# Performance work log

Hardware: AMD Instinct MI355X
Metric: run time of the kernel (lower is better)

## Reference

```python
import jax, jax.numpy as jnp
import numpy as np

N_NODES = 50000
N_EDGES = 600000
N_LABEL = 200000
IN_CH = 128
OUT_CH = 128
K_HOPS = 2


def setup_inputs() -> dict:
    key = jax.random.key(0)
    ks = jax.random.split(key, 9)
    x = jax.random.normal(ks[0], (N_NODES, IN_CH), dtype=jnp.float32)
    edge_index = jax.random.randint(ks[1], (2, N_EDGES), 0, N_NODES)
    edge_label_index = jax.random.randint(ks[2], (2, N_LABEL), 0, N_NODES)
    conv_weight = jax.random.normal(ks[3], (OUT_CH, IN_CH), dtype=jnp.float32) * 0.05
    conv_bias = jax.random.normal(ks[4], (OUT_CH,), dtype=jnp.float32) * 0.05
    w1 = jax.random.normal(ks[5], (OUT_CH // 2, OUT_CH), dtype=jnp.float32) * 0.05
    b1 = jax.random.normal(ks[6], (OUT_CH // 2,), dtype=jnp.float32) * 0.05
    w2 = jax.random.normal(ks[7], (1, OUT_CH // 2), dtype=jnp.float32) * 0.05
    b2 = jax.random.normal(ks[8], (1,), dtype=jnp.float32) * 0.05
    return {"x": x, "edge_index": edge_index, "edge_label_index": edge_label_index,
            "conv_weight": conv_weight, "conv_bias": conv_bias,
            "w1": w1, "b1": b1, "w2": w2, "b2": b2}


def reference(x, edge_index, edge_label_index, conv_weight, conv_bias, w1, b1, w2, b2):
    n = x.shape[0]
    # gcn_norm with self-loops: A_hat = D^{-1/2} (A + I) D^{-1/2}
    loop = jnp.arange(n, dtype=edge_index.dtype)
    src = jnp.concatenate([edge_index[0], loop])  # message sources
    dst = jnp.concatenate([edge_index[1], loop])  # aggregation targets
    deg = jax.ops.segment_sum(jnp.ones_like(dst, dtype=x.dtype), dst, num_segments=n)
    dinv = jnp.where(deg > 0, jax.lax.rsqrt(deg), 0.0)
    w = dinv[src] * dinv[dst]  # [E+N] edge weights

    # K-hop propagation: h <- A_hat h, repeated K times (SGConv)
    h = x
    for _ in range(K_HOPS):
        h = jax.ops.segment_sum(h[src] * w[:, None], dst, num_segments=n)
    z = h @ conv_weight.T + conv_bias  # [N, out_channels]

    # decode: gather endpoint embeddings, multiply, tiny MLP (dropout inactive at eval)
    s = z[edge_label_index[0]] * z[edge_label_index[1]]  # [E_label, out]
    h1 = jax.nn.relu(s @ w1.T + b1)
    r = (h1 @ w2.T + b2).sum(axis=-1)  # [E_label]
    return r
```

## Files before the change

### kernel.cpp

```cpp
#include <hip/hip_runtime.h>

#define N_CH 128

typedef _Float16 half8  __attribute__((ext_vector_type(8)));
typedef _Float16 half4v __attribute__((ext_vector_type(4)));
typedef float    floatx4 __attribute__((ext_vector_type(4)));


__global__ void k_prep(int* __restrict__ cnt,
                       const float* __restrict__ W,  _Float16* __restrict__ wh,
                       const float* __restrict__ W1, _Float16* __restrict__ w1h,
                       int n) {
    int i = blockIdx.x * blockDim.x + threadIdx.x;
    if (i < n) cnt[i] = 0;
    int nw4  = N_CH * N_CH / 4;
    int nw14 = 64 * N_CH / 4;
    if (i < nw4) {
        float4 v = ((const float4*)W)[i];
        half4v o;
        o[0] = (_Float16)v.x; o[1] = (_Float16)v.y; o[2] = (_Float16)v.z; o[3] = (_Float16)v.w;
        ((half4v*)wh)[i] = o;
    } else if (i < nw4 + nw14) {
        int j = i - nw4;
        float4 v = ((const float4*)W1)[j];
        half4v o;
        o[0] = (_Float16)v.x; o[1] = (_Float16)v.y; o[2] = (_Float16)v.z; o[3] = (_Float16)v.w;
        ((half4v*)w1h)[j] = o;
    }
}


__global__ void k_count(const int* __restrict__ dst, int* __restrict__ cnt, int E) {
    int e = blockIdx.x * blockDim.x + threadIdx.x;
    if (e < E) atomicAdd(&cnt[dst[e]], 1);
}

__global__ __launch_bounds__(1024) void k_scan1(const int* __restrict__ cnt,
                                                int* __restrict__ offs,
                                                int* __restrict__ bsum, int n) {
    __shared__ int ssum[16];
    int tid = threadIdx.x;
    int lane = tid & 63, wid = tid >> 6;
    int i = blockIdx.x * 1024 + tid;
    int v = (i < n) ? cnt[i] : 0;
    int x = v;
    #pragma unroll
    for (int off = 1; off < 64; off <<= 1) {
        int y = __shfl_up(x, off, 64);
        if (lane >= off) x += y;
    }
    if (lane == 63) ssum[wid] = x;
    __syncthreads();
    if (wid == 0 && lane < 16) {
        int s = ssum[lane];
        #pragma unroll
        for (int off = 1; off < 16; off <<= 1) {
            int y = __shfl_up(s, off, 64);
            if (lane >= off) s += y;
        }
        ssum[lane] = s;
    }
    __syncthreads();
    int waveoff = (wid > 0) ? ssum[wid - 1] : 0;
    int incl = x + waveoff;
    if (i < n) offs[i] = incl - v;
    if (tid == 1023) bsum[blockIdx.x] = incl;
}

__global__ __launch_bounds__(64) void k_scan2(const int* __restrict__ bsum,
                                              int* __restrict__ bbase, int nb) {
    int lane = threadIdx.x;
    int v = (lane < nb) ? bsum[lane] : 0;
    int x = v;
    #pragma unroll
    for (int off = 1; off < 64; off <<= 1) {
        int y = __shfl_up(x, off, 64);
        if (lane >= off) x += y;
    }
    if (lane < nb) bbase[lane] = x - v;
}

__global__ void k_scan3(const int* __restrict__ cnt, int* __restrict__ offs,
                        const int* __restrict__ bbase, int* __restrict__ cur,
                        float* __restrict__ dinv, int n) {
    int i = blockIdx.x * blockDim.x + threadIdx.x;
    if (i < n) {
        int o = offs[i] + bbase[i >> 10];
        offs[i] = o;
        cur[i]  = o;
        dinv[i] = rsqrtf((float)(cnt[i] + 1));
    }
}

__global__ void k_fill(const int* __restrict__ src, const int* __restrict__ dst,
                       int* __restrict__ cur, unsigned short* __restrict__ csr, int E) {
    int e = blockIdx.x * blockDim.x + threadIdx.x;
    if (e < E) {
        int p = atomicAdd(&cur[dst[e]], 1);
        csr[p] = (unsigned short)src[e];
    }
}


__global__ void k_scale(const float* __restrict__ x, const float* __restrict__ dinv,
                        _Float16* __restrict__ u0, _Float16* __restrict__ u1, int n) {
    int i = blockIdx.x * blockDim.x + threadIdx.x;
    int nx4 = n * (N_CH / 4);
    if (i < nx4) {
        float d = dinv[i >> 5];
        float4 v = ((const float4*)x)[i];
        half4v o;
        o[0] = (_Float16)(d * v.x); o[1] = (_Float16)(d * v.y);
        o[2] = (_Float16)(d * v.z); o[3] = (_Float16)(d * v.w);
        ((half4v*)u0)[i] = o;
    } else if (i < nx4 + 64) {
        int j = i - nx4;
        half4v zz; zz[0] = (_Float16)0.f; zz[1] = (_Float16)0.f; zz[2] = (_Float16)0.f; zz[3] = (_Float16)0.f;
        _Float16* dst16 = (j < 32) ? u0 : u1;
        ((half4v*)(dst16 + (size_t)n * N_CH))[j & 31] = zz;
    }
}


__global__ __launch_bounds__(256) void k_hop16(const _Float16* __restrict__ hin,
                                               _Float16* __restrict__ hout,
                                               const int* __restrict__ offs,
                                               const int* __restrict__ cnt,
                                               const float* __restrict__ dinv,
                                               const unsigned short* __restrict__ csr,
                                               int n, int squared) {
    int tid  = threadIdx.x;
    int node = blockIdx.x * 16 + (tid >> 4);
    int c16  = tid & 15;
    if (node >= n) return;
    float di = dinv[node];
    float sc = squared ? di * di : di;
    int s0 = offs[node], c = cnt[node];
    const unsigned short* lst = csr + s0;
    half8 self = ((const half8*)(hin + (size_t)node * N_CH))[c16];
    float acc[8];
    #pragma unroll
    for (int j = 0; j < 8; ++j) acc[j] = (float)self[j];
    for (int t0 = 0; t0 < c; t0 += 8) {
        int idx[8];
        #pragma unroll
        for (int i = 0; i < 8; ++i) {
            int t = t0 + i;
            unsigned short v = lst[t];
            idx[i] = (t < c) ? (int)v : n;
        }
        half8 u[8];
        #pragma unroll
        for (int i = 0; i < 8; ++i)
            u[i] = ((const half8*)(hin + (size_t)idx[i] * N_CH))[c16];
        #pragma unroll
        for (int i = 0; i < 8; ++i)
            #pragma unroll
            for (int j = 0; j < 8; ++j) acc[j] += (float)u[i][j];
    }
    half8 o;
    #pragma unroll
    for (int j = 0; j < 8; ++j) o[j] = (_Float16)(sc * acc[j]);
    ((half8*)(hout + (size_t)node * N_CH))[c16] = o;
}


__global__ __launch_bounds__(256) void k_zlin_mfma(const _Float16* __restrict__ h,
                                                   const _Float16* __restrict__ wh,
                                                   const float* __restrict__ bc,
                                                   _Float16* __restrict__ z, int n) {
    __shared__ half8 wls[128 * 16];
    int tid = threadIdx.x;
    int lane = tid & 63, w = tid >> 6;
    int quad = lane >> 4, m16 = lane & 15;
    int nb = blockIdx.x * 64;
    #pragma unroll
    for (int i = 0; i < 8; ++i) {
        int g = tid + 256 * i;
        int r = g >> 4, c = g & 15;
        wls[r * 16 + (c ^ (r & 15))] = ((const half8*)wh)[g];
    }
    int arow = nb + w * 16 + m16;
    const half8* hrow = (const half8*)(h + (size_t)arow * N_CH);
    half8 a[4];
    #pragma unroll
    for (int kk = 0; kk < 4; ++kk) a[kk] = hrow[kk * 4 + quad];
    __syncthreads();
    int outnode0 = nb + w * 16 + quad * 4;
    #pragma unroll
    for (int jt = 0; jt < 8; ++jt) {
        floatx4 acc = {0.f, 0.f, 0.f, 0.f};
        #pragma unroll
        for (int kk = 0; kk < 4; ++kk) {
            int r = jt * 16 + m16;
            half8 bfr = wls[r * 16 + ((kk * 4 + quad) ^ m16)];
            acc = __builtin_amdgcn_mfma_f32_16x16x32_f16(a[kk], bfr, acc, 0, 0, 0);
        }
        int j = jt * 16 + m16;
        float bias = bc[j];
        #pragma unroll
        for (int reg = 0; reg < 4; ++reg) {
            int node = outnode0 + reg;
            if (node < n) z[(size_t)node * N_CH + j] = (_Float16)(acc[reg] + bias);
        }
    }
}


__global__ __launch_bounds__(256) void k_decode_mfma(const _Float16* __restrict__ z,
        const int* __restrict__ ai, const int* __restrict__ bi,
        const _Float16* __restrict__ w1h, const float* __restrict__ b1,
        const float* __restrict__ w2, const float* __restrict__ b2,
        float* __restrict__ out, int m) {
    __shared__ half8 w1ls[64 * 16];
    __shared__ half8 sls[64 * 16];
    int tid = threadIdx.x;
    int lane = tid & 63, w = tid >> 6;
    int quad = lane >> 4, m16 = lane & 15;
    int pbase = blockIdx.x * 64;
    #pragma unroll
    for (int i = 0; i < 4; ++i) {
        int g = tid + 256 * i;
        int r = g >> 4, c = g & 15;
        w1ls[r * 16 + (c ^ (r & 15))] = ((const half8*)w1h)[g];
    }
    int pidx = pbase + w * 16 + m16;
    if (pidx >= m) pidx = m - 1;
    int idxa = ai[pidx];
    int idxb = bi[pidx];
    int ia[4], ib[4];
    #pragma unroll
    for (int it = 0; it < 4; ++it) {
        int p = it * 4 + quad;
        ia[it] = __shfl(idxa, p, 64);
        ib[it] = __shfl(idxb, p, 64);
    }
    half8 za[4], zb[4];
    #pragma unroll
    for (int it = 0; it < 4; ++it) {
        za[it] = ((const half8*)(z + (size_t)ia[it] * N_CH))[m16];
        zb[it] = ((const half8*)(z + (size_t)ib[it] * N_CH))[m16];
    }
    #pragma unroll
    for (int it = 0; it < 4; ++it) {
        half8 s8 = za[it] * zb[it];
        int pp = w * 16 + it * 4 + quad;
        sls[pp * 16 + (m16 ^ (pp & 15))] = s8;
    }
    __syncthreads();
    half8 a[4];
    #pragma unroll
    for (int kk = 0; kk < 4; ++kk)
        a[kk] = sls[(w * 16 + m16) * 16 + ((kk * 4 + quad) ^ m16)];
    float rsum[4] = {0.f, 0.f, 0.f, 0.f};
    #pragma unroll
    for (int jt = 0; jt < 4; ++jt) {
        floatx4 acc = {0.f, 0.f, 0.f, 0.f};
        #pragma unroll
        for (int kk = 0; kk < 4; ++kk) {
            int r = jt * 16 + m16;
            half8 bfr = w1ls[r * 16 + ((kk * 4 + quad) ^ m16)];
            acc = __builtin_amdgcn_mfma_f32_16x16x32_f16(a[kk], bfr, acc, 0, 0, 0);
        }
        int j = jt * 16 + m16;
        float b1j = b1[j], w2j = w2[j];
        #pragma unroll
        for (int reg = 0; reg < 4; ++reg) {
            float v = fmaxf(acc[reg] + b1j, 0.f) * w2j;
            v += __shfl_xor(v, 1, 64);
            v += __shfl_xor(v, 2, 64);
            v += __shfl_xor(v, 4, 64);
            v += __shfl_xor(v, 8, 64);
            rsum[reg] += v;
        }
    }
    if (m16 == 0) {
        float bb = b2[0];
        #pragma unroll
        for (int reg = 0; reg < 4; ++reg) {
            int gp = pbase + w * 16 + quad * 4 + reg;
            if (gp < m) out[gp] = rsum[reg] + bb;
        }
    }
}


extern "C" void kernel_launch(void* const* d_in, const int* in_sizes, int n_in,
                              void* d_out, int out_size, void* d_ws, size_t ws_size,
                              hipStream_t stream) {
    const float* x   = (const float*)d_in[0];
    const int*   ei  = (const int*)d_in[1];
    const int*   eli = (const int*)d_in[2];
    const float* W   = (const float*)d_in[3];
    const float* bc  = (const float*)d_in[4];
    const float* W1  = (const float*)d_in[5];
    const float* b1  = (const float*)d_in[6];
    const float* w2  = (const float*)d_in[7];
    const float* b2  = (const float*)d_in[8];
    float* out = (float*)d_out;

    const int N = in_sizes[0] / N_CH;
    const int E = in_sizes[1] / 2;
    const int M = in_sizes[2] / 2;

    const int* src = ei;
    const int* dst = ei + E;
    const int* ai  = eli;
    const int* bi  = eli + M;

    _Float16* hb0 = (_Float16*)d_ws;
    _Float16* hb1 = hb0 + (size_t)(N + 1) * N_CH;
    _Float16* wh  = hb1 + (size_t)(N + 1) * N_CH;
    _Float16* w1h = wh + 16384;
    unsigned short* csr = (unsigned short*)(w1h + 8192);
    int*   cnt  = (int*)(csr + E);
    int*   off  = cnt + N;
    int*   cur  = off + N;
    float* dnv  = (float*)(cur + N);
    int*   bsum = (int*)(dnv + N);
    int*   bbas = bsum + 64;

    int nb = (N + 1023) / 1024;
    k_prep<<<(N + 255) / 256, 256, 0, stream>>>(cnt, W, wh, W1, w1h, N);
    k_count<<<(E + 255) / 256, 256, 0, stream>>>(dst, cnt, E);
    k_scan1<<<nb, 1024, 0, stream>>>(cnt, off, bsum, N);
    k_scan2<<<1, 64, 0, stream>>>(bsum, bbas, nb);
    k_scan3<<<(N + 255) / 256, 256, 0, stream>>>(cnt, off, bbas, cur, dnv, N);
    k_fill<<<(E + 255) / 256, 256, 0, stream>>>(src, dst, cur, csr, E);
    int sc_work = N * (N_CH / 4) + 64;
    k_scale<<<(sc_work + 255) / 256, 256, 0, stream>>>(x, dnv, hb0, hb1, N);

    int hop_blocks = (N + 15) / 16;
    k_hop16<<<hop_blocks, 256, 0, stream>>>(hb0, hb1, off, cnt, dnv, csr, N, 1);
    k_hop16<<<hop_blocks, 256, 0, stream>>>(hb1, hb0, off, cnt, dnv, csr, N, 0);

    k_zlin_mfma<<<(N + 63) / 64, 256, 0, stream>>>(hb0, wh, bc, hb1, N);

    k_decode_mfma<<<(M + 63) / 64, 256, 0, stream>>>(hb1, ai, bi, w1h, b1, w2, b2, out, M);
}
```

Before: 232.3 us.

## Pad CSR rows to multiples of eight and fuse block-scan into scan3

Each node's CSR adjacency list is padded to a multiple of 8 entries, with the padding filled with a dummy zero-row index. The hop kernel can then fetch indices as aligned 16-byte uint4 loads, prefetch the next group, and drop the per-element bounds check. The single-block k_scan2 launch is folded into k_scan3, where every block redoes the 64-entry block-sum scan in shared memory. The cost is a larger CSR buffer, extra gathers of the dummy row for padded slots, and a redundant small scan in every block.

```diff
diff --git a/kernel.cpp b/kernel.cpp
--- a/kernel.cpp
+++ b/kernel.cpp
@@ -42,7 +42,7 @@
     int tid = threadIdx.x;
     int lane = tid & 63, wid = tid >> 6;
     int i = blockIdx.x * 1024 + tid;
-    int v = (i < n) ? cnt[i] : 0;
+    int v = (i < n) ? ((cnt[i] + 7) & ~7) : 0;
     int x = v;
     #pragma unroll
     for (int off = 1; off < 64; off <<= 1) {
@@ -67,28 +67,36 @@
     if (tid == 1023) bsum[blockIdx.x] = incl;
 }
 
-__global__ __launch_bounds__(64) void k_scan2(const int* __restrict__ bsum,
-                                              int* __restrict__ bbase, int nb) {
-    int lane = threadIdx.x;
-    int v = (lane < nb) ? bsum[lane] : 0;
-    int x = v;
-    #pragma unroll
-    for (int off = 1; off < 64; off <<= 1) {
-        int y = __shfl_up(x, off, 64);
-        if (lane >= off) x += y;
-    }
-    if (lane < nb) bbase[lane] = x - v;
-}
-
-__global__ void k_scan3(const int* __restrict__ cnt, int* __restrict__ offs,
-                        const int* __restrict__ bbase, int* __restrict__ cur,
-                        float* __restrict__ dinv, int n) {
-    int i = blockIdx.x * blockDim.x + threadIdx.x;
+__global__ __launch_bounds__(256) void k_scan3(const int* __restrict__ cnt,
+                                               int* __restrict__ offs,
+                                               const int* __restrict__ bsum,
+                                               int* __restrict__ cur,
+                                               float* __restrict__ dinv,
+                                               unsigned short* __restrict__ csr,
+                                               int n, int nb) {
+    __shared__ int sbb[64];
+    int tid = threadIdx.x;
+    if (tid < 64) {
+        int v = (tid < nb) ? bsum[tid] : 0;
+        int x = v;
+        #pragma unroll
+        for (int off = 1; off < 64; off <<= 1) {
+            int y = __shfl_up(x, off, 64);
+            if (tid >= off) x += y;
+        }
+        sbb[tid] = x - v;
+    }
+    __syncthreads();
+    int i = blockIdx.x * blockDim.x + tid;
     if (i < n) {
-        int o = offs[i] + bbase[i >> 10];
+        int o = offs[i] + sbb[i >> 10];
         offs[i] = o;
         cur[i]  = o;
-        dinv[i] = rsqrtf((float)(cnt[i] + 1));
+        int c = cnt[i];
+        dinv[i] = rsqrtf((float)(c + 1));
+        int cp = (c + 7) & ~7;
+        unsigned short zn = (unsigned short)n;
+        for (int j = c; j < cp; ++j) csr[o + j] = zn;
     }
 }
 
@@ -135,20 +143,24 @@
     if (node >= n) return;
     float di = dinv[node];
     float sc = squared ? di * di : di;
-    int s0 = offs[node], c = cnt[node];
-    const unsigned short* lst = csr + s0;
+    int s0 = offs[node];
+    int cp = (cnt[node] + 7) & ~7;
+    const uint4* qlst = (const uint4*)(csr + s0);
     half8 self = ((const half8*)(hin + (size_t)node * N_CH))[c16];
     float acc[8];
     #pragma unroll
     for (int j = 0; j < 8; ++j) acc[j] = (float)self[j];
-    for (int t0 = 0; t0 < c; t0 += 8) {
+    int nq = cp >> 3;
+    uint4 pk;
+    if (nq > 0) pk = qlst[0];
+    for (int q = 0; q < nq; ++q) {
+        uint4 cpk = pk;
+        if (q + 1 < nq) pk = qlst[q + 1];
         int idx[8];
-        #pragma unroll
-        for (int i = 0; i < 8; ++i) {
-            int t = t0 + i;
-            unsigned short v = lst[t];
-            idx[i] = (t < c) ? (int)v : n;
-        }
+        idx[0] = cpk.x & 0xFFFF; idx[1] = cpk.x >> 16;
+        idx[2] = cpk.y & 0xFFFF; idx[3] = cpk.y >> 16;
+        idx[4] = cpk.z & 0xFFFF; idx[5] = cpk.z >> 16;
+        idx[6] = cpk.w & 0xFFFF; idx[7] = cpk.w >> 16;
         half8 u[8];
         #pragma unroll
         for (int i = 0; i < 8; ++i)
@@ -313,19 +325,17 @@
     _Float16* wh  = hb1 + (size_t)(N + 1) * N_CH;
     _Float16* w1h = wh + 16384;
     unsigned short* csr = (unsigned short*)(w1h + 8192);
-    int*   cnt  = (int*)(csr + E);
+    int*   cnt  = (int*)(csr + (size_t)E + 8 * (size_t)N);
     int*   off  = cnt + N;
     int*   cur  = off + N;
     float* dnv  = (float*)(cur + N);
     int*   bsum = (int*)(dnv + N);
-    int*   bbas = bsum + 64;
 
     int nb = (N + 1023) / 1024;
     k_prep<<<(N + 255) / 256, 256, 0, stream>>>(cnt, W, wh, W1, w1h, N);
     k_count<<<(E + 255) / 256, 256, 0, stream>>>(dst, cnt, E);
     k_scan1<<<nb, 1024, 0, stream>>>(cnt, off, bsum, N);
-    k_scan2<<<1, 64, 0, stream>>>(bsum, bbas, nb);
-    k_scan3<<<(N + 255) / 256, 256, 0, stream>>>(cnt, off, bbas, cur, dnv, N);
+    k_scan3<<<(N + 255) / 256, 256, 0, stream>>>(cnt, off, bsum, cur, dnv, csr, N, nb);
     k_fill<<<(E + 255) / 256, 256, 0, stream>>>(src, dst, cur, csr, E);
     int sc_work = N * (N_CH / 4) + 64;
     k_scale<<<(sc_work + 255) / 256, 256, 0, stream>>>(x, dnv, hb0, hb1, N);
```

Result: no change. 233.6 us (+0.6%).
